# Kernel optimization log

Measured on AMD Instinct MI355X. Metric: run time of the kernel, lower is better.

The kernel has to match this reference:

```python
import jax, jax.numpy as jnp
import numpy as np

B = 1048576          # batch size
ALPHA1, ALPHA2, ALPHA3 = 1.2566, 1.5, 0.9
S_STAR = 20.0
TAU = 4.0


def _f_matrix(a1, a2, a3):
    # fixed 6x6 dynamics matrix built by the i in {1,2} loop in CBF_Parameters
    f = jnp.zeros((6, 6), jnp.float32)
    f = f.at[2, 1].set(1.0).at[2, 3].set(-1.0)
    f = f.at[3, 1].set(a3).at[3, 2].set(a1).at[3, 3].set(-a2)
    f = f.at[4, 3].set(1.0).at[4, 5].set(-1.0)
    f = f.at[5, 3].set(a3).at[5, 4].set(a1).at[5, 5].set(-a2)
    return f


def setup_inputs() -> dict:
    key = jax.random.key(0)
    ks = jax.random.split(key, 7)
    z = jax.random.normal(ks[0], (B, 6), jnp.float32)
    tilde_vh = jnp.zeros((1,), jnp.float32)  # unused in forward (dead code in source)
    W1 = jax.random.normal(ks[1], (50, 6), jnp.float32) * 0.3
    b1 = jax.random.normal(ks[2], (50,), jnp.float32) * 0.1
    W2 = jax.random.normal(ks[3], (100, 50), jnp.float32) * 0.1
    b2 = jax.random.normal(ks[4], (100,), jnp.float32) * 0.1
    W3 = jax.random.normal(ks[5], (5, 100), jnp.float32) * 0.1
    b3 = jax.random.normal(ks[6], (5,), jnp.float32) * 0.1
    return dict(z=z, tilde_vh=tilde_vh, W1=W1, b1=b1, W2=W2, b2=b2, W3=W3, b3=b3)


def reference(z, tilde_vh, W1, b1, W2, b2, W3, b3):
    # tiny MLP, no activations (faithful to fc3(fc2(fc1(z))))
    u = ((z @ W1.T + b1) @ W2.T + b2) @ W3.T + b3        # (B, 5)
    p1, p2, p3 = u[:, 1], u[:, 2], u[:, 3]

    # faithful: torch reshape (row-major reinterpret), not transpose
    X = z.reshape(6, -1)                                  # (6, B)
    f = _f_matrix(ALPHA1, ALPHA2, ALPHA3)
    fX = f @ X                                            # (6, B)

    # index == 2 constraint (while loop body never runs: delta_b[1]=tau != 0)
    d2 = jnp.zeros(6, jnp.float32).at[1].set(TAU).at[2].set(1.0).at[3].set(-TAU)
    eta1 = X[2] + S_STAR - TAU * (X[3] - X[1])            # (B,)
    bb1 = d2 @ fX + p1 * eta1                             # (B,)

    # index == 3 constraint (while loop runs exactly once: d3[1]==0 -> d3u[1]=tau*alpha3)
    d3 = jnp.zeros(6, jnp.float32).at[3].set(TAU).at[4].set(1.0).at[5].set(-TAU)
    d3u = d3 @ f                                          # one f-multiplication
    eta2a = X[4] + S_STAR - TAU * (X[5] - X[3])           # (B,)
    eta2b = d3u @ X                                       # (B,)
    bb2 = d3u @ fX + p2 * eta2a + p3 * eta2b              # (B,)

    A = jnp.stack([-d2[1], -d3u[1]])                      # (2,) constraint normals
    h = jnp.stack([bb1, bb2], axis=1)                     # (B, 2)

    # per-sample 1-D QP: min 0.25*x^2 - u0*x  s.t. A_i * x <= h_i  (Q = 0.5)
    x_unc = 2.0 * u[:, 0]
    ratios = h / A                                        # (B, 2)
    neg_inf = jnp.float32(-1e30)
    pos_inf = jnp.float32(1e30)
    lb = jnp.max(jnp.where(A < 0, ratios, neg_inf), axis=1)
    ub = jnp.min(jnp.where(A > 0, ratios, pos_inf), axis=1)
    return jnp.clip(x_unc, lb, ub)[:, None]               # (B, 1)
```

## Files before the change

### kernel.cpp

```cpp
#include <hip/hip_runtime.h>

#define ALPHA1 1.2566f
#define ALPHA2 1.5f
#define ALPHA3 0.9f
#define S_STAR 20.0f
#define TAU    4.0f

__global__ __launch_bounds__(256) void setup_kernel(
        const float* __restrict__ W1, const float* __restrict__ b1,
        const float* __restrict__ W2, const float* __restrict__ b2,
        const float* __restrict__ W3, const float* __restrict__ b3,
        float* __restrict__ ws) {
    __shared__ float T[100][6];
    __shared__ float c2[100];
    const int tid = threadIdx.x;

    for (int idx = tid; idx < 600; idx += blockDim.x) {
        const int i = idx / 6, k = idx % 6;
        float s = 0.f;
        #pragma unroll 10
        for (int h = 0; h < 50; ++h) s += W2[i * 50 + h] * W1[h * 6 + k];
        T[i][k] = s;
    }
    for (int i = tid; i < 100; i += blockDim.x) {
        float s = b2[i];
        #pragma unroll 10
        for (int h = 0; h < 50; ++h) s += W2[i * 50 + h] * b1[h];
        c2[i] = s;
    }
    __syncthreads();
    for (int idx = tid; idx < 30; idx += blockDim.x) {
        const int m = idx / 6, k = idx % 6;
        float s = 0.f;
        #pragma unroll 10
        for (int i = 0; i < 100; ++i) s += W3[m * 100 + i] * T[i][k];
        ws[idx] = s;
    }
    for (int m = tid; m < 5; m += blockDim.x) {
        float s = b3[m];
        #pragma unroll 10
        for (int i = 0; i < 100; ++i) s += W3[m * 100 + i] * c2[i];
        ws[30 + m] = s;
    }
}

__global__ __launch_bounds__(256) void main_kernel(
        const float* __restrict__ z, const float* __restrict__ ws,
        float* __restrict__ out, int B4, long long B) {
    const long long t = (long long)blockIdx.x * blockDim.x + threadIdx.x;
    if (t >= B4) return;
    const long long j0 = t * 4;

    float M[4][6], c[4];
    #pragma unroll
    for (int m = 0; m < 4; ++m) {
        #pragma unroll
        for (int k = 0; k < 6; ++k) M[m][k] = ws[m * 6 + k];
        c[m] = ws[30 + m];
    }

    float zz[24];
    const float4* zr = (const float4*)(z + j0 * 6);
    #pragma unroll
    for (int v = 0; v < 6; ++v) {
        const float4 q = zr[v];
        zz[4 * v + 0] = q.x; zz[4 * v + 1] = q.y;
        zz[4 * v + 2] = q.z; zz[4 * v + 3] = q.w;
    }

    float X[6][4];
    #pragma unroll
    for (int i = 0; i < 6; ++i) {
        const float4 q = *(const float4*)(z + (long long)i * B + j0);
        X[i][0] = q.x; X[i][1] = q.y; X[i][2] = q.z; X[i][3] = q.w;
    }

    const float g1 = TAU * ALPHA3;
    const float g2 = TAU * ALPHA1;
    const float g3 = 1.f - TAU * ALPHA2 - TAU * ALPHA3;
    const float g4 = -TAU * ALPHA1;
    const float g5 = TAU * ALPHA2 - 1.f;

    float4 o;
    float* op = &o.x;
    #pragma unroll
    for (int r = 0; r < 4; ++r) {
        float u[4];
        #pragma unroll
        for (int m = 0; m < 4; ++m) {
            float s = c[m];
            #pragma unroll
            for (int k = 0; k < 6; ++k) s = fmaf(M[m][k], zz[r * 6 + k], s);
            u[m] = s;
        }
        const float x1 = X[1][r], x2 = X[2][r], x3 = X[3][r];
        const float x4 = X[4][r], x5 = X[5][r];

        const float fx2 = x1 - x3;
        const float fx3 = ALPHA3 * x1 + ALPHA1 * x2 - ALPHA2 * x3;
        const float fx4 = x3 - x5;
        const float fx5 = ALPHA3 * x3 + ALPHA1 * x4 - ALPHA2 * x5;

        const float eta1 = x2 + S_STAR - TAU * (x3 - x1);
        const float bb1  = (fx2 - TAU * fx3) + u[1] * eta1;

        const float eta2a = x4 + S_STAR - TAU * (x5 - x3);
        const float eta2b = g1 * x1 + g2 * x2 + g3 * x3 + g4 * x4 + g5 * x5;
        const float d3ufX = g2 * fx2 + g3 * fx3 + g4 * fx4 + g5 * fx5;
        const float bb2   = d3ufX + u[2] * eta2a + u[3] * eta2b;

        const float r1 = bb1 / (-TAU);
        const float r2 = bb2 / (-(TAU * ALPHA3));
        const float lb = fmaxf(r1, r2);
        const float xu = 2.f * u[0];
        op[r] = fminf(fmaxf(xu, lb), 1e30f);
    }
    *(float4*)(out + j0) = o;
}

extern "C" void kernel_launch(void* const* d_in, const int* in_sizes, int n_in,
                              void* d_out, int out_size, void* d_ws, size_t ws_size,
                              hipStream_t stream) {
    const float* z  = (const float*)d_in[0];
    const float* W1 = (const float*)d_in[2];
    const float* b1 = (const float*)d_in[3];
    const float* W2 = (const float*)d_in[4];
    const float* b2 = (const float*)d_in[5];
    const float* W3 = (const float*)d_in[6];
    const float* b3 = (const float*)d_in[7];
    float* out = (float*)d_out;
    float* ws  = (float*)d_ws;

    const long long B = (long long)in_sizes[0] / 6;

    setup_kernel<<<1, 256, 0, stream>>>(W1, b1, W2, b2, W3, b3, ws);

    const int B4 = (int)(B / 4);
    const int threads = 256;
    const int blocks = (B4 + threads - 1) / threads;
    main_kernel<<<blocks, threads, 0, stream>>>(z, ws, out, B4, B);
}
```

Before: 96.83 us.

## Fuse weight-collapse setup into main kernel with per-block recompute

Removes the separate single-block setup kernel and has every block redundantly collapse the three-layer linear MLP into a 4x6 matrix and bias in shared memory. The association is changed to W3*W2 first, then times W1, so only rows 0-3 are computed. Each thread now handles two groups of four samples, which halves the block count. This drops a kernel launch and the serial dependency on a one-block kernel, but adds about 100-iteration dot products per block that run before streaming, plus two barriers. The grid size assumes B divides evenly by 2048 and there is no bounds guard.

```diff
diff --git a/kernel.cpp b/kernel.cpp
--- a/kernel.cpp
+++ b/kernel.cpp
@@ -6,73 +6,54 @@
 #define S_STAR 20.0f
 #define TAU    4.0f
 
-__global__ __launch_bounds__(256) void setup_kernel(
+constexpr int TPB = 256;
+
+__global__ __launch_bounds__(TPB) void fused_kernel(
+        const float* __restrict__ z,
         const float* __restrict__ W1, const float* __restrict__ b1,
         const float* __restrict__ W2, const float* __restrict__ b2,
         const float* __restrict__ W3, const float* __restrict__ b3,
-        float* __restrict__ ws) {
-    __shared__ float T[100][6];
-    __shared__ float c2[100];
+        float* __restrict__ out, long long B) {
+    __shared__ float Vs[4][52];
+    __shared__ float Ms[4][6];
+    __shared__ float cs[4];
     const int tid = threadIdx.x;
 
-    for (int idx = tid; idx < 600; idx += blockDim.x) {
-        const int i = idx / 6, k = idx % 6;
+    if (tid < 200) {
+        const int m = tid / 50, h = tid % 50;
         float s = 0.f;
         #pragma unroll 10
-        for (int h = 0; h < 50; ++h) s += W2[i * 50 + h] * W1[h * 6 + k];
-        T[i][k] = s;
-    }
-    for (int i = tid; i < 100; i += blockDim.x) {
-        float s = b2[i];
-        #pragma unroll 10
-        for (int h = 0; h < 50; ++h) s += W2[i * 50 + h] * b1[h];
-        c2[i] = s;
+        for (int i = 0; i < 100; ++i)
+            s = fmaf(W3[m * 100 + i], W2[i * 50 + h], s);
+        Vs[m][h] = s;
     }
     __syncthreads();
-    for (int idx = tid; idx < 30; idx += blockDim.x) {
-        const int m = idx / 6, k = idx % 6;
+    if (tid < 24) {
+        const int m = tid / 6, k = tid % 6;
         float s = 0.f;
         #pragma unroll 10
-        for (int i = 0; i < 100; ++i) s += W3[m * 100 + i] * T[i][k];
-        ws[idx] = s;
-    }
-    for (int m = tid; m < 5; m += blockDim.x) {
+        for (int h = 0; h < 50; ++h)
+            s = fmaf(Vs[m][h], W1[h * 6 + k], s);
+        Ms[m][k] = s;
+    } else if (tid < 28) {
+        const int m = tid - 24;
         float s = b3[m];
         #pragma unroll 10
-        for (int i = 0; i < 100; ++i) s += W3[m * 100 + i] * c2[i];
-        ws[30 + m] = s;
+        for (int i = 0; i < 100; ++i)
+            s = fmaf(W3[m * 100 + i], b2[i], s);
+        #pragma unroll 10
+        for (int h = 0; h < 50; ++h)
+            s = fmaf(Vs[m][h], b1[h], s);
+        cs[m] = s;
     }
-}
-
-__global__ __launch_bounds__(256) void main_kernel(
-        const float* __restrict__ z, const float* __restrict__ ws,
-        float* __restrict__ out, int B4, long long B) {
-    const long long t = (long long)blockIdx.x * blockDim.x + threadIdx.x;
-    if (t >= B4) return;
-    const long long j0 = t * 4;
+    __syncthreads();
 
     float M[4][6], c[4];
     #pragma unroll
     for (int m = 0; m < 4; ++m) {
         #pragma unroll
-        for (int k = 0; k < 6; ++k) M[m][k] = ws[m * 6 + k];
-        c[m] = ws[30 + m];
-    }
-
-    float zz[24];
-    const float4* zr = (const float4*)(z + j0 * 6);
-    #pragma unroll
-    for (int v = 0; v < 6; ++v) {
-        const float4 q = zr[v];
-        zz[4 * v + 0] = q.x; zz[4 * v + 1] = q.y;
-        zz[4 * v + 2] = q.z; zz[4 * v + 3] = q.w;
-    }
-
-    float X[6][4];
-    #pragma unroll
-    for (int i = 0; i < 6; ++i) {
-        const float4 q = *(const float4*)(z + (long long)i * B + j0);
-        X[i][0] = q.x; X[i][1] = q.y; X[i][2] = q.z; X[i][3] = q.w;
+        for (int k = 0; k < 6; ++k) M[m][k] = Ms[m][k];
+        c[m] = cs[m];
     }
 
     const float g1 = TAU * ALPHA3;
@@ -81,41 +62,63 @@
     const float g4 = -TAU * ALPHA1;
     const float g5 = TAU * ALPHA2 - 1.f;
 
-    float4 o;
-    float* op = &o.x;
     #pragma unroll
-    for (int r = 0; r < 4; ++r) {
-        float u[4];
+    for (int s2 = 0; s2 < 2; ++s2) {
+        const long long j0 =
+            ((long long)blockIdx.x * (2 * TPB) + s2 * TPB + tid) * 4;
+
+        float zz[24];
+        const float4* zr = (const float4*)(z + j0 * 6);
         #pragma unroll
-        for (int m = 0; m < 4; ++m) {
-            float s = c[m];
+        for (int v = 0; v < 6; ++v) {
+            const float4 q = zr[v];
+            zz[4 * v + 0] = q.x; zz[4 * v + 1] = q.y;
+            zz[4 * v + 2] = q.z; zz[4 * v + 3] = q.w;
+        }
+
+        float X[6][4];
+        #pragma unroll
+        for (int i = 0; i < 6; ++i) {
+            const float4 q = *(const float4*)(z + (long long)i * B + j0);
+            X[i][0] = q.x; X[i][1] = q.y; X[i][2] = q.z; X[i][3] = q.w;
+        }
+
+        float4 o;
+        float* op = &o.x;
+        #pragma unroll
+        for (int r = 0; r < 4; ++r) {
+            float u[4];
             #pragma unroll
-            for (int k = 0; k < 6; ++k) s = fmaf(M[m][k], zz[r * 6 + k], s);
-            u[m] = s;
+            for (int m = 0; m < 4; ++m) {
+                float s = c[m];
+                #pragma unroll
+                for (int k = 0; k < 6; ++k) s = fmaf(M[m][k], zz[r * 6 + k], s);
+                u[m] = s;
+            }
+            const float x1 = X[1][r], x2 = X[2][r], x3 = X[3][r];
+            const float x4 = X[4][r], x5 = X[5][r];
+
+            const float fx2 = x1 - x3;
+            const float fx3 = ALPHA3 * x1 + ALPHA1 * x2 - ALPHA2 * x3;
+            const float fx4 = x3 - x5;
+            const float fx5 = ALPHA3 * x3 + ALPHA1 * x4 - ALPHA2 * x5;
+
+            const float eta1 = x2 + S_STAR - TAU * (x3 - x1);
+            const float bb1  = (fx2 - TAU * fx3) + u[1] * eta1;
+
+            const float eta2a = x4 + S_STAR - TAU * (x5 - x3);
+            const float eta2b = g1 * x1 + g2 * x2 + g3 * x3 + g4 * x4 + g5 * x5;
+            const float d3ufX = g2 * fx2 + g3 * fx3 + g4 * fx4 + g5 * fx5;
+            const float bb2   = d3ufX + u[2] * eta2a + u[3] * eta2b;
+
+            const float r1 = bb1 / (-TAU);
+            const float r2 = bb2 / (-(TAU * ALPHA3));
+            const float lb = fmaxf(r1, r2);
+            const float xu = 2.f * u[0];
+            op[r] = fminf(fmaxf(xu, lb), 1e30f);
         }
-        const float x1 = X[1][r], x2 = X[2][r], x3 = X[3][r];
-        const float x4 = X[4][r], x5 = X[5][r];
-
-        const float fx2 = x1 - x3;
-        const float fx3 = ALPHA3 * x1 + ALPHA1 * x2 - ALPHA2 * x3;
-        const float fx4 = x3 - x5;
-        const float fx5 = ALPHA3 * x3 + ALPHA1 * x4 - ALPHA2 * x5;
-
-        const float eta1 = x2 + S_STAR - TAU * (x3 - x1);
-        const float bb1  = (fx2 - TAU * fx3) + u[1] * eta1;
-
-        const float eta2a = x4 + S_STAR - TAU * (x5 - x3);
-        const float eta2b = g1 * x1 + g2 * x2 + g3 * x3 + g4 * x4 + g5 * x5;
-        const float d3ufX = g2 * fx2 + g3 * fx3 + g4 * fx4 + g5 * fx5;
-        const float bb2   = d3ufX + u[2] * eta2a + u[3] * eta2b;
-
-        const float r1 = bb1 / (-TAU);
-        const float r2 = bb2 / (-(TAU * ALPHA3));
-        const float lb = fmaxf(r1, r2);
-        const float xu = 2.f * u[0];
-        op[r] = fminf(fmaxf(xu, lb), 1e30f);
+        *(float4*)(out + j0) = o;
     }
-    *(float4*)(out + j0) = o;
 }
 
 extern "C" void kernel_launch(void* const* d_in, const int* in_sizes, int n_in,
@@ -129,14 +132,9 @@
     const float* W3 = (const float*)d_in[6];
     const float* b3 = (const float*)d_in[7];
     float* out = (float*)d_out;
-    float* ws  = (float*)d_ws;
 
     const long long B = (long long)in_sizes[0] / 6;
 
-    setup_kernel<<<1, 256, 0, stream>>>(W1, b1, W2, b2, W3, b3, ws);
-
-    const int B4 = (int)(B / 4);
-    const int threads = 256;
-    const int blocks = (B4 + threads - 1) / threads;
-    main_kernel<<<blocks, threads, 0, stream>>>(z, ws, out, B4, B);
+    const int blocks = (int)(B / (4LL * 2 * TPB));
+    fused_kernel<<<blocks, TPB, 0, stream>>>(z, W1, b1, W2, b2, W3, b3, out, B);
 }
```

Measured after the change: 93.05 us. 1.04x faster.
